# Optimization experiments

Hardware: AMD Instinct MI355X
Metric: run time of the kernel (lower is better)

Reference implementation:

```python
import jax, jax.numpy as jnp
import numpy as np

B, S, D = 2, 2048, 2048
H = 16
DH = D // H  # 128, head dim for q, also the single kv head dim
ROPE_BASE = 10000.0


def _rope_cos_sin(seq_len, dim, dtype):
    inv_freq = 1.0 / (ROPE_BASE ** (jnp.arange(0, dim, 2, dtype=jnp.float32) / dim))
    t = jnp.arange(seq_len, dtype=jnp.float32)
    freqs = jnp.outer(t, inv_freq)            # [S, dim/2]
    emb = jnp.concatenate([freqs, freqs], -1)  # [S, dim]
    return jnp.cos(emb).astype(dtype), jnp.sin(emb).astype(dtype)


def _rotate_half(x):
    x1, x2 = x[..., : x.shape[-1] // 2], x[..., x.shape[-1] // 2 :]
    return jnp.concatenate([-x2, x1], axis=-1)


def setup_inputs() -> dict:
    key = jax.random.key(0)
    ks = jax.random.split(key, 7)
    s = 0.02
    return {
        "x": jax.random.normal(ks[0], (B, S, D), jnp.float32),
        "q_weight": jax.random.normal(ks[1], (H * DH, D), jnp.float32) * s,
        "q_bias": jax.random.normal(ks[2], (H * DH,), jnp.float32) * s,
        "kv_weight": jax.random.normal(ks[3], (2 * DH, D), jnp.float32) * s,
        "kv_bias": jax.random.normal(ks[4], (2 * DH,), jnp.float32) * s,
        "o_weight": jax.random.normal(ks[5], (D, H * DH), jnp.float32) * s,
        "o_bias": jax.random.normal(ks[6], (D,), jnp.float32) * s,
    }


def reference(x, q_weight, q_bias, kv_weight, kv_bias, o_weight, o_bias):
    b, s, d = x.shape
    # fused-style MQA projections (torch F.linear: y = x @ W.T + b)
    q = x @ q_weight.T + q_bias                      # [B,S,H*DH]
    kv = x @ kv_weight.T + kv_bias                   # [B,S,2*DH]
    q = q.reshape(b, s, H, DH)
    k, v = kv[..., :DH], kv[..., DH:]                # [B,S,DH] single kv head

    # rotary embedding (GPT-NeoX / rotate_half style) on q and k
    cos, sin = _rope_cos_sin(s, DH, x.dtype)         # [S,DH]
    q = q * cos[None, :, None, :] + _rotate_half(q) * sin[None, :, None, :]
    k = k * cos[None, :, :] + _rotate_half(k) * sin[None, :, :]

    # causal MQA attention (flash_attn_varlen with full masks == dense causal)
    scale = 1.0 / jnp.sqrt(jnp.asarray(DH, x.dtype))
    scores = jnp.einsum("bqhd,bkd->bhqk", q, k) * scale   # [B,H,S,S]
    causal = jnp.tril(jnp.ones((s, s), bool))
    scores = jnp.where(causal[None, None], scores, jnp.asarray(-1e9, x.dtype))
    probs = jax.nn.softmax(scores, axis=-1)
    attn = jnp.einsum("bhqk,bkd->bqhd", probs, v)         # [B,S,H,DH]

    out = attn.reshape(b, s, H * DH) @ o_weight.T + o_bias
    return out
```

## Files before the change

kernel.cpp:

```cpp
#include <hip/hip_runtime.h>
#include <math.h>

constexpr int Bb  = 2;
constexpr int Ss  = 2048;
constexpr int Dd  = 2048;
constexpr int Hh  = 16;
constexpr int DHd = 128;
constexpr int BS  = Bb * Ss;
constexpr int NQKV = 2304;

typedef __bf16 bf16x8 __attribute__((ext_vector_type(8)));
typedef float  f32x4  __attribute__((ext_vector_type(4)));

static __device__ __forceinline__ unsigned short f2bf(float f) {
  union { float f; unsigned int u; } a; a.f = f;
  unsigned int u = a.u;
  unsigned int r = (u + 0x7fffu + ((u >> 16) & 1u)) >> 16;
  return (unsigned short)r;
}
static __device__ __forceinline__ float bf2f(unsigned short u) {
  union { unsigned int u; float f; } a; a.u = ((unsigned int)u) << 16;
  return a.f;
}
static __device__ __forceinline__ int cvtpk(float lo, float hi) {
  int r;
  asm("v_cvt_pk_bf16_f32 %0, %1, %2" : "=v"(r) : "v"(lo), "v"(hi));
  return r;
}
static __device__ __forceinline__ f32x4 mfma16(bf16x8 a, bf16x8 b, f32x4 c) {
  return __builtin_amdgcn_mfma_f32_16x16x32_bf16(a, b, c, 0, 0, 0);
}

__global__ __launch_bounds__(256) void cast_all(
    const float* __restrict__ qw, const float* __restrict__ kvw,
    const float* __restrict__ ow, const float* __restrict__ x,
    unsigned short* __restrict__ dst,
    float2* __restrict__ ctab)
{
  const int blk = blockIdx.x;
  if (blk >= 16896) {
    const int id = (blk - 16896) * 256 + threadIdx.x;
    const int s = id >> 6, i = id & 63;
    const float invf = exp2f(-(float)i * (13.287712379549449f / 64.0f));
    const float ang = (float)s * invf;
    ctab[id] = make_float2(cosf(ang), sinf(ang));
    return;
  }
  const int i = blk * 256 + threadIdx.x;
  const float* src; int off;
  if (i < 1048576)      { src = qw;  off = 0; }
  else if (i < 1179648) { src = kvw; off = 1048576; }
  else if (i < 2228224) { src = ow;  off = 1179648; }
  else                  { src = x;   off = 2228224; }
  const float4 v = ((const float4*)src)[i - off];
  ushort4 o;
  o.x = f2bf(v.x); o.y = f2bf(v.y); o.z = f2bf(v.z); o.w = f2bf(v.w);
  ((ushort4*)dst)[i] = o;
}

#define TM 128
#define TN 128
#define TK 32

#define GLOAD16(gp, lp)                                                        \
  __builtin_amdgcn_global_load_lds(                                            \
      (const __attribute__((address_space(1))) void*)(gp),                     \
      (__attribute__((address_space(3))) void*)(lp), 16, 0, 0)

template <bool BF16OUT>
__global__ __launch_bounds__(256) void gemm_bt_mfma(
    const unsigned short* __restrict__ A,
    const unsigned short* __restrict__ Bw,
    const float* __restrict__ bias1,
    const float* __restrict__ bias2,
    int nsplit,
    void* __restrict__ Cv,
    int M, int N, int K)
{
  __shared__ unsigned short As[TM * TK];
  __shared__ unsigned short Bs[TN * TK];

  const int tid  = threadIdx.x;
  const int w    = tid >> 6;
  const int lane = tid & 63;
  const int m0   = blockIdx.y * TM;
  const int n0   = blockIdx.x * TN;
  const int wm   = (w >> 1) * 64;
  const int wn   = (w & 1) * 64;

  f32x4 acc[4][4];
#pragma unroll
  for (int i = 0; i < 4; i++)
#pragma unroll
    for (int j = 0; j < 4; j++) acc[i][j] = (f32x4){0.f, 0.f, 0.f, 0.f};

  const int srow = lane >> 2;
  const int scol = (lane & 3) * 8;
  const unsigned short* aG0 = A  + (size_t)(m0 +      w * 16 + srow) * K + scol;
  const unsigned short* aG1 = A  + (size_t)(m0 + 64 + w * 16 + srow) * K + scol;
  const unsigned short* bG0 = Bw + (size_t)(n0 +      w * 16 + srow) * K + scol;
  const unsigned short* bG1 = Bw + (size_t)(n0 + 64 + w * 16 + srow) * K + scol;
  unsigned short* aL0 = &As[(     w * 16) * TK];
  unsigned short* aL1 = &As[(64 + w * 16) * TK];
  unsigned short* bL0 = &Bs[(     w * 16) * TK];
  unsigned short* bL1 = &Bs[(64 + w * 16) * TK];

  const int fr = lane & 15;
  const int fk = (lane >> 4) * 8;

  for (int k0 = 0; k0 < K; k0 += TK) {
    __syncthreads();
    GLOAD16(aG0 + k0, aL0);
    GLOAD16(aG1 + k0, aL1);
    GLOAD16(bG0 + k0, bL0);
    GLOAD16(bG1 + k0, bL1);
    __syncthreads();

    bf16x8 af[4], bfr[4];
#pragma unroll
    for (int i = 0; i < 4; i++)
      af[i] = *(const bf16x8*)&As[(wm + i * 16 + fr) * TK + fk];
#pragma unroll
    for (int j = 0; j < 4; j++)
      bfr[j] = *(const bf16x8*)&Bs[(wn + j * 16 + fr) * TK + fk];
#pragma unroll
    for (int i = 0; i < 4; i++)
#pragma unroll
      for (int j = 0; j < 4; j++)
        acc[i][j] = mfma16(af[i], bfr[j], acc[i][j]);
  }

  const int er = (lane >> 4) * 4;
  const int ec = lane & 15;
#pragma unroll
  for (int j = 0; j < 4; j++) {
    const int col = n0 + wn + j * 16 + ec;
    const float bv = (col < nsplit) ? bias1[col] : bias2[col - nsplit];
#pragma unroll
    for (int i = 0; i < 4; i++) {
      const int rbase = m0 + wm + i * 16 + er;
#pragma unroll
      for (int r = 0; r < 4; r++) {
        const float v = acc[i][j][r] + bv;
        if constexpr (BF16OUT)
          ((unsigned short*)Cv)[(size_t)(rbase + r) * N + col] = f2bf(v);
        else
          ((float*)Cv)[(size_t)(rbase + r) * N + col] = v;
      }
    }
  }
}

__global__ __launch_bounds__(256) void prep_kv(
    const unsigned short* __restrict__ QKV,
    const float2* __restrict__ ctab,
    unsigned short* __restrict__ Kb,
    unsigned short* __restrict__ Vt)
{
  __shared__ unsigned short Vtile[64 * 136];

  const int blk = blockIdx.x;
  const int b   = blk >> 5;
  const int s0  = (blk & 31) * 64;
  const int t   = threadIdx.x;

  {
    const int r = t >> 2, p = t & 3;
    const int row = blk * 64 + r;
    const int s = row & (Ss - 1);
    const unsigned short* src = QKV + (size_t)row * NQKV + 2048 + p * 16;
    const float2* ct = ctab + s * 64 + p * 16;
    union { uint4 v[2]; unsigned short a[16]; } lo, hi, ol, oh;
    lo.v[0] = *(const uint4*)src;        lo.v[1] = *(const uint4*)(src + 8);
    hi.v[0] = *(const uint4*)(src + 64); hi.v[1] = *(const uint4*)(src + 72);
#pragma unroll
    for (int e = 0; e < 16; e++) {
      const float2 cs = ct[e];
      const float l = bf2f(lo.a[e]), hh = bf2f(hi.a[e]);
      ol.a[e] = f2bf(l * cs.x - hh * cs.y);
      oh.a[e] = f2bf(hh * cs.x + l * cs.y);
    }
    unsigned short* dst = Kb + (size_t)row * 128 + p * 16;
    *(uint4*)dst        = ol.v[0]; *(uint4*)(dst + 8)  = ol.v[1];
    *(uint4*)(dst + 64) = oh.v[0]; *(uint4*)(dst + 72) = oh.v[1];
  }

#pragma unroll
  for (int c = 0; c < 4; c++) {
    const int id = c * 256 + t;
    const int vr = id >> 4, cc = id & 15;
    *(uint4*)&Vtile[vr * 136 + cc * 8] =
        *(const uint4*)(QKV + (size_t)(blk * 64 + vr) * NQKV + 2176 + cc * 8);
  }
  __syncthreads();

  {
    const int d = t >> 1, half = t & 1;
    union { uint4 v[4]; unsigned short a[32]; } val;
#pragma unroll
    for (int kk = 0; kk < 32; kk++)
      val.a[kk] = Vtile[(half * 32 + kk) * 136 + d];
    unsigned short* dst = Vt + ((size_t)(b * 128 + d)) * Ss + s0 + half * 32;
#pragma unroll
    for (int c = 0; c < 4; c++) *(uint4*)(dst + c * 8) = val.v[c];
  }
}

__global__ __launch_bounds__(256, 2) void flash_v11(
    const unsigned short* __restrict__ QKV,
    const unsigned short* __restrict__ Kb,
    const unsigned short* __restrict__ Vt,
    const float2* __restrict__ ctab,
    unsigned short* __restrict__ attn)
{
  __shared__ unsigned short Ks[4 * 128 * 32];
  __shared__ unsigned short Vs[4 * 128 * 32];

  const int g  = (int)blockIdx.x;
  const int lo = g & 255, hi = g >> 8;
  const int p  = hi ? (15 - (lo & 15)) : (lo & 15);
  const int hb = (lo >> 4) + 16 * hi;
  const int h  = hb & 15;
  const int b  = hb >> 4;

  const int qA0 = (31 - p) * 64;
  const int qB0 = p * 64;

  const int tid = threadIdx.x;
  const int w = tid >> 6, lane = tid & 63;
  const int lg = lane >> 4, lm = lane & 15;
  const int qrowA = qA0 + w * 16 + lm;
  const int qrowA_lo = qA0 + w * 16;
  const int qrowA_hi = qA0 + w * 16 + 15;
  const int qrowB = qB0 + w * 16 + lm;
  const int qrowB_lo = qB0 + w * 16;
  const int qrowB_hi = qB0 + w * 16 + 15;

  const int klg = lg ^ ((lm >> 1) & 3);

  const float sscale = 0.08838834764831845f * 1.4426950408889634f;

  bf16x8 qfA[4], qfB[4];
  {
    union U8 { bf16x8 v; unsigned short a[8]; };
#pragma unroll
    for (int tile = 0; tile < 2; tile++) {
      const int qrow = tile ? qrowB : qrowA;
      const unsigned short* qp =
          QKV + (size_t)(b * Ss + qrow) * NQKV + h * DHd + lg * 8;
      const float2* ct = ctab + qrow * 64 + lg * 8;
      U8 lo0, lo1, hi0, hi1, ol0, ol1, oh0, oh1;
      lo0.v = *(const bf16x8*)(qp);
      lo1.v = *(const bf16x8*)(qp + 32);
      hi0.v = *(const bf16x8*)(qp + 64);
      hi1.v = *(const bf16x8*)(qp + 96);
#pragma unroll
      for (int j = 0; j < 8; j++) {
        {
          const float2 cs = ct[j];
          const float l = bf2f(lo0.a[j]), hh = bf2f(hi0.a[j]);
          ol0.a[j] = f2bf((l * cs.x - hh * cs.y) * sscale);
          oh0.a[j] = f2bf((hh * cs.x + l * cs.y) * sscale);
        }
        {
          const float2 cs = ct[32 + j];
          const float l = bf2f(lo1.a[j]), hh = bf2f(hi1.a[j]);
          ol1.a[j] = f2bf((l * cs.x - hh * cs.y) * sscale);
          oh1.a[j] = f2bf((hh * cs.x + l * cs.y) * sscale);
        }
      }
      if (tile == 0) { qfA[0]=ol0.v; qfA[1]=ol1.v; qfA[2]=oh0.v; qfA[3]=oh1.v; }
      else           { qfB[0]=ol0.v; qfB[1]=ol1.v; qfB[2]=oh0.v; qfB[3]=oh1.v; }
    }
  }

  f32x4 otA[8], otB[8];
#pragma unroll
  for (int dt = 0; dt < 8; dt++) {
    otA[dt] = (f32x4){0.f, 0.f, 0.f, 0.f};
    otB[dt] = (f32x4){0.f, 0.f, 0.f, 0.f};
  }
  float lsumA = 0.f, lsumB = 0.f;

  const int sr  = lane >> 2;
  const int sc8 = ((lane & 3) ^ ((lane >> 3) & 3)) * 8;
  const unsigned short* kg =
      Kb + (size_t)b * Ss * 128 + (size_t)sr * 128 + w * 32 + sc8;
  const unsigned short* vg =
      Vt + (size_t)b * 128 * Ss + (size_t)(w * 32 + sr) * Ss + sc8;
  unsigned short* ksl = &Ks[w * 4096];

  const int addr0 = (2 * (lg & 1)) * 16 + lm;
  const int addr1 = addr0 + 16;
  const bool sel_hi = (lg & 2) != 0;

  auto half32 = [&](int keybase, int tA, const unsigned short* VsP,
                    const bf16x8 (&qf)[4], f32x4 (&ot)[8], float& lsum,
                    int qrow, bool needmask) {
    f32x4 s[2];
    s[0] = (f32x4){0.f, 0.f, 0.f, 0.f};
    s[1] = (f32x4){0.f, 0.f, 0.f, 0.f};
    __builtin_amdgcn_s_setprio(1);
#pragma unroll
    for (int kf = 0; kf < 4; kf++) {
      const bf16x8 k0 = *(const bf16x8*)&Ks[kf * 4096 + ((tA)     * 16 + lm) * 32 + klg * 8];
      const bf16x8 k1 = *(const bf16x8*)&Ks[kf * 4096 + ((tA + 1) * 16 + lm) * 32 + klg * 8];
      s[0] = mfma16(k0, qf[kf], s[0]);
      s[1] = mfma16(k1, qf[kf], s[1]);
    }
    __builtin_amdgcn_s_setprio(0);
    int pk[2][2];
#pragma unroll
    for (int t = 0; t < 2; t++) {
      float pv[4];
#pragma unroll
      for (int r = 0; r < 4; r++) pv[r] = exp2f(s[t][r]);
      if (needmask) {
        const int kb = keybase + t * 16 + 4 * lg;
#pragma unroll
        for (int r = 0; r < 4; r++)
          if (kb + r > qrow) pv[r] = 0.f;
      }
#pragma unroll
      for (int r = 0; r < 4; r++) lsum += pv[r];
      pk[t][0] = cvtpk(pv[0], pv[1]);
      pk[t][1] = cvtpk(pv[2], pv[3]);
    }
    union { int d[4]; bf16x8 v; } pb;
#pragma unroll
    for (int d = 0; d < 4; d++) {
      const int src = (d < 2) ? addr0 : addr1;
      const int v0 = __shfl(pk[0][d & 1], src);
      const int v1 = __shfl(pk[1][d & 1], src);
      pb.d[d] = sel_hi ? v1 : v0;
    }
    __builtin_amdgcn_s_setprio(1);
#pragma unroll
    for (int dt = 0; dt < 8; dt++) {
      const bf16x8 vfrag = *(const bf16x8*)&VsP[(dt * 16 + lm) * 32 + klg * 8];
      ot[dt] = mfma16(vfrag, pb.v, ot[dt]);
    }
    __builtin_amdgcn_s_setprio(0);
  };

  for (int j0 = 0; j0 <= qA0; j0 += 128) {
    __syncthreads();
#pragma unroll
    for (int i = 0; i < 8; i++)
      GLOAD16(kg + (size_t)(j0 + i * 16) * 128, ksl + i * 512);
#pragma unroll
    for (int ks2 = 0; ks2 < 4; ks2++) {
      unsigned short* vsl = &Vs[ks2 * 4096 + (w * 32) * 32];
      GLOAD16(vg + j0 + ks2 * 32,                  vsl);
      GLOAD16(vg + (size_t)16 * Ss + j0 + ks2 * 32, vsl + 512);
    }
    __syncthreads();

#pragma unroll
    for (int t32 = 0; t32 < 4; t32++) {
      const int kb = j0 + t32 * 32;
      if (kb <= qrowA_hi)
        half32(kb, t32 * 2, &Vs[t32 * 4096], qfA, otA, lsumA, qrowA,
               kb + 31 > qrowA_lo);
    }
#pragma unroll
    for (int t32 = 0; t32 < 4; t32++) {
      const int kb = j0 + t32 * 32;
      if (kb <= qrowB_hi)
        half32(kb, t32 * 2, &Vs[t32 * 4096], qfB, otB, lsumB, qrowB,
               kb + 31 > qrowB_lo);
    }
  }

#pragma unroll
  for (int tile = 0; tile < 2; tile++) {
    float lsum = tile ? lsumB : lsumA;
    const int qrow = tile ? qrowB : qrowA;
    lsum += __shfl_xor(lsum, 16);
    lsum += __shfl_xor(lsum, 32);
    const float inv = 1.0f / lsum;
    unsigned short* dst =
        attn + (size_t)(b * Ss + qrow) * Dd + h * DHd + lg * 4;
#pragma unroll
    for (int dt = 0; dt < 8; dt++) {
      const f32x4 o = tile ? otB[dt] : otA[dt];
      uint2 st;
      st.x = (unsigned int)cvtpk(o[0] * inv, o[1] * inv);
      st.y = (unsigned int)cvtpk(o[2] * inv, o[3] * inv);
      *(uint2*)(dst + dt * 16) = st;
    }
  }
}

extern "C" void kernel_launch(void* const* d_in, const int* in_sizes, int n_in,
                              void* d_out, int out_size, void* d_ws, size_t ws_size,
                              hipStream_t stream) {
  const float* x   = (const float*)d_in[0];
  const float* qw  = (const float*)d_in[1];
  const float* qb  = (const float*)d_in[2];
  const float* kvw = (const float*)d_in[3];
  const float* kvb = (const float*)d_in[4];
  const float* ow  = (const float*)d_in[5];
  const float* ob  = (const float*)d_in[6];
  float* out = (float*)d_out;

  unsigned short* wsb    = (unsigned short*)d_ws;
  unsigned short* wqkv   = wsb;
  unsigned short* owb    = wsb + 4718592;
  unsigned short* xb     = wsb + 8912896;
  unsigned short* attn_b = xb;
  unsigned short* QKV    = wsb + 17301504;
  unsigned short* Kb     = wsb + 26738688;
  unsigned short* Vt     = wsb + 27262976;
  float2*         ctab   = (float2*)(wsb + 27787264);

  cast_all<<<17408, 256, 0, stream>>>(qw, kvw, ow, x, wqkv, ctab);

  gemm_bt_mfma<true><<<dim3(NQKV / TN, BS / TM), 256, 0, stream>>>(
      xb, wqkv, qb, kvb, 2048, QKV, BS, NQKV, Dd);

  prep_kv<<<BS / 64, 256, 0, stream>>>(QKV, ctab, Kb, Vt);

  flash_v11<<<512, 256, 0, stream>>>(QKV, Kb, Vt, ctab, attn_b);

  gemm_bt_mfma<false><<<dim3(Dd / TN, BS / TM), 256, 0, stream>>>(
      attn_b, owb, ob, ob, Dd, out, BS, Dd, Dd);
}
```

Measured before the change: 304.3 us.

## Double-buffer K/V tiles in flash attention with 64-key prefetch pipeline

Splits the attention key loop into 64-key tiles held in two shared-memory buffers. The next tile's K and V global-to-LDS loads are issued right after the barrier, so they overlap with the MFMA work on the current tile, and each iteration needs one barrier instead of two. A new tile64_2 path handles both 32-key halves together, with four score MFMAs interleaved per k-fragment, and falls back to half32 on the diagonal edge. In exchange the loop runs twice as many iterations, shared-memory use and register pressure go up, and correctness depends on the barrier also waiting for the outstanding loads.

```diff
diff --git a/kernel.cpp b/kernel.cpp
--- a/kernel.cpp
+++ b/kernel.cpp
@@ -206,15 +206,15 @@
   }
 }
 
-__global__ __launch_bounds__(256, 2) void flash_v11(
+__global__ __launch_bounds__(256, 2) void flash_v12(
     const unsigned short* __restrict__ QKV,
     const unsigned short* __restrict__ Kb,
     const unsigned short* __restrict__ Vt,
     const float2* __restrict__ ctab,
     unsigned short* __restrict__ attn)
 {
-  __shared__ unsigned short Ks[4 * 128 * 32];
-  __shared__ unsigned short Vs[4 * 128 * 32];
+  __shared__ unsigned short Ks[2 * 8192];
+  __shared__ unsigned short Vs[2 * 8192];
 
   const int g  = (int)blockIdx.x;
   const int lo = g & 255, hi = g >> 8;
@@ -288,27 +288,41 @@
       Kb + (size_t)b * Ss * 128 + (size_t)sr * 128 + w * 32 + sc8;
   const unsigned short* vg =
       Vt + (size_t)b * 128 * Ss + (size_t)(w * 32 + sr) * Ss + sc8;
-  unsigned short* ksl = &Ks[w * 4096];
+
+  auto stage = [&](int bi, int jj) {
+    unsigned short* ksl  = &Ks[bi * 8192 + w * 2048];
+    unsigned short* vsl0 = &Vs[bi * 8192 + (w * 32) * 32];
+    unsigned short* vsl1 = &Vs[bi * 8192 + 4096 + (w * 32) * 32];
+#pragma unroll
+    for (int i = 0; i < 4; i++)
+      GLOAD16(kg + (size_t)(jj + i * 16) * 128, ksl + i * 512);
+#pragma unroll
+    for (int i = 0; i < 2; i++) {
+      GLOAD16(vg + (size_t)(i * 16) * Ss + jj,      vsl0 + i * 512);
+      GLOAD16(vg + (size_t)(i * 16) * Ss + jj + 32, vsl1 + i * 512);
+    }
+  };
 
   const int addr0 = (2 * (lg & 1)) * 16 + lm;
   const int addr1 = addr0 + 16;
   const bool sel_hi = (lg & 2) != 0;
 
-  auto half32 = [&](int keybase, int tA, const unsigned short* VsP,
-                    const bf16x8 (&qf)[4], f32x4 (&ot)[8], float& lsum,
-                    int qrow, bool needmask) {
+  auto half32 = [&](const unsigned short* KsB, const unsigned short* VsB,
+                    int keybase, const bf16x8 (&qf)[4], f32x4 (&ot)[8],
+                    float& lsum, int qrow, int qrow_lo) {
     f32x4 s[2];
     s[0] = (f32x4){0.f, 0.f, 0.f, 0.f};
     s[1] = (f32x4){0.f, 0.f, 0.f, 0.f};
     __builtin_amdgcn_s_setprio(1);
 #pragma unroll
     for (int kf = 0; kf < 4; kf++) {
-      const bf16x8 k0 = *(const bf16x8*)&Ks[kf * 4096 + ((tA)     * 16 + lm) * 32 + klg * 8];
-      const bf16x8 k1 = *(const bf16x8*)&Ks[kf * 4096 + ((tA + 1) * 16 + lm) * 32 + klg * 8];
+      const bf16x8 k0 = *(const bf16x8*)&KsB[kf * 2048 + (      lm) * 32 + klg * 8];
+      const bf16x8 k1 = *(const bf16x8*)&KsB[kf * 2048 + (16 + lm) * 32 + klg * 8];
       s[0] = mfma16(k0, qf[kf], s[0]);
       s[1] = mfma16(k1, qf[kf], s[1]);
     }
     __builtin_amdgcn_s_setprio(0);
+    const bool needmask = keybase + 31 > qrow_lo;
     int pk[2][2];
 #pragma unroll
     for (int t = 0; t < 2; t++) {
@@ -337,39 +351,98 @@
     __builtin_amdgcn_s_setprio(1);
 #pragma unroll
     for (int dt = 0; dt < 8; dt++) {
-      const bf16x8 vfrag = *(const bf16x8*)&VsP[(dt * 16 + lm) * 32 + klg * 8];
-      ot[dt] = mfma16(vfrag, pb.v, ot[dt]);
+      const bf16x8 vf = *(const bf16x8*)&VsB[(dt * 16 + lm) * 32 + klg * 8];
+      ot[dt] = mfma16(vf, pb.v, ot[dt]);
     }
     __builtin_amdgcn_s_setprio(0);
   };
 
-  for (int j0 = 0; j0 <= qA0; j0 += 128) {
+  auto tile64_2 = [&](const unsigned short* KsB, const unsigned short* VsB,
+                      int keybase, const bf16x8 (&qf)[4], f32x4 (&ot)[8],
+                      float& lsum, int qrow, int qrow_lo) {
+    f32x4 s[2][2];
+#pragma unroll
+    for (int hf = 0; hf < 2; hf++) {
+      s[hf][0] = (f32x4){0.f, 0.f, 0.f, 0.f};
+      s[hf][1] = (f32x4){0.f, 0.f, 0.f, 0.f};
+    }
+    __builtin_amdgcn_s_setprio(1);
+#pragma unroll
+    for (int kf = 0; kf < 4; kf++) {
+      const bf16x8 k00 = *(const bf16x8*)&KsB[kf * 2048 + (      lm) * 32 + klg * 8];
+      const bf16x8 k01 = *(const bf16x8*)&KsB[kf * 2048 + (16 + lm) * 32 + klg * 8];
+      const bf16x8 k10 = *(const bf16x8*)&KsB[kf * 2048 + (32 + lm) * 32 + klg * 8];
+      const bf16x8 k11 = *(const bf16x8*)&KsB[kf * 2048 + (48 + lm) * 32 + klg * 8];
+      s[0][0] = mfma16(k00, qf[kf], s[0][0]);
+      s[0][1] = mfma16(k01, qf[kf], s[0][1]);
+      s[1][0] = mfma16(k10, qf[kf], s[1][0]);
+      s[1][1] = mfma16(k11, qf[kf], s[1][1]);
+    }
+    __builtin_amdgcn_s_setprio(0);
+    int pk[2][2][2];
+#pragma unroll
+    for (int hf = 0; hf < 2; hf++) {
+      const bool needmask = keybase + hf * 32 + 31 > qrow_lo;
+#pragma unroll
+      for (int t = 0; t < 2; t++) {
+        float pv[4];
+#pragma unroll
+        for (int r = 0; r < 4; r++) pv[r] = exp2f(s[hf][t][r]);
+        if (needmask) {
+          const int kb = keybase + hf * 32 + t * 16 + 4 * lg;
+#pragma unroll
+          for (int r = 0; r < 4; r++)
+            if (kb + r > qrow) pv[r] = 0.f;
+        }
+#pragma unroll
+        for (int r = 0; r < 4; r++) lsum += pv[r];
+        pk[hf][t][0] = cvtpk(pv[0], pv[1]);
+        pk[hf][t][1] = cvtpk(pv[2], pv[3]);
+      }
+    }
+    union { int d[4]; bf16x8 v; } pb[2];
+#pragma unroll
+    for (int hf = 0; hf < 2; hf++) {
+#pragma unroll
+      for (int d = 0; d < 4; d++) {
+        const int src = (d < 2) ? addr0 : addr1;
+        const int v0 = __shfl(pk[hf][0][d & 1], src);
+        const int v1 = __shfl(pk[hf][1][d & 1], src);
+        pb[hf].d[d] = sel_hi ? v1 : v0;
+      }
+    }
+    __builtin_amdgcn_s_setprio(1);
+#pragma unroll
+    for (int dt = 0; dt < 8; dt++) {
+      const bf16x8 vf0 = *(const bf16x8*)&VsB[       (dt * 16 + lm) * 32 + klg * 8];
+      const bf16x8 vf1 = *(const bf16x8*)&VsB[4096 + (dt * 16 + lm) * 32 + klg * 8];
+      ot[dt] = mfma16(vf0, pb[0].v, ot[dt]);
+      ot[dt] = mfma16(vf1, pb[1].v, ot[dt]);
+    }
+    __builtin_amdgcn_s_setprio(0);
+  };
+
+  stage(0, 0);
+  int cur = 0;
+  for (int j0 = 0; j0 <= qA0; j0 += 64) {
     __syncthreads();
-#pragma unroll
-    for (int i = 0; i < 8; i++)
-      GLOAD16(kg + (size_t)(j0 + i * 16) * 128, ksl + i * 512);
-#pragma unroll
-    for (int ks2 = 0; ks2 < 4; ks2++) {
-      unsigned short* vsl = &Vs[ks2 * 4096 + (w * 32) * 32];
-      GLOAD16(vg + j0 + ks2 * 32,                  vsl);
-      GLOAD16(vg + (size_t)16 * Ss + j0 + ks2 * 32, vsl + 512);
-    }
-    __syncthreads();
-
-#pragma unroll
-    for (int t32 = 0; t32 < 4; t32++) {
-      const int kb = j0 + t32 * 32;
-      if (kb <= qrowA_hi)
-        half32(kb, t32 * 2, &Vs[t32 * 4096], qfA, otA, lsumA, qrowA,
-               kb + 31 > qrowA_lo);
-    }
-#pragma unroll
-    for (int t32 = 0; t32 < 4; t32++) {
-      const int kb = j0 + t32 * 32;
-      if (kb <= qrowB_hi)
-        half32(kb, t32 * 2, &Vs[t32 * 4096], qfB, otB, lsumB, qrowB,
-               kb + 31 > qrowB_lo);
-    }
+    if (j0 + 64 <= qA0) stage(cur ^ 1, j0 + 64);
+
+    const unsigned short* KsB = &Ks[cur * 8192];
+    const unsigned short* VsB = &Vs[cur * 8192];
+
+    if (j0 + 32 <= qrowA_hi)
+      tile64_2(KsB, VsB, j0, qfA, otA, lsumA, qrowA, qrowA_lo);
+    else
+      half32(KsB, VsB, j0, qfA, otA, lsumA, qrowA, qrowA_lo);
+
+    if (j0 <= qrowB_hi) {
+      if (j0 + 32 <= qrowB_hi)
+        tile64_2(KsB, VsB, j0, qfB, otB, lsumB, qrowB, qrowB_lo);
+      else
+        half32(KsB, VsB, j0, qfB, otB, lsumB, qrowB, qrowB_lo);
+    }
+    cur ^= 1;
   }
 
 #pragma unroll
@@ -421,7 +494,7 @@
 
   prep_kv<<<BS / 64, 256, 0, stream>>>(QKV, ctab, Kb, Vt);
 
-  flash_v11<<<512, 256, 0, stream>>>(QKV, Kb, Vt, ctab, attn_b);
+  flash_v12<<<512, 256, 0, stream>>>(QKV, Kb, Vt, ctab, attn_b);
 
   gemm_bt_mfma<false><<<dim3(Dd / TN, BS / TM), 256, 0, stream>>>(
       attn_b, owb, ob, ob, Dd, out, BS, Dd, Dd);
```

New measurement: 305.4 us. Within noise of the previous version (+0.4%).

## Split paired query tiles across separate waves in 512-thread flash blocks

Applied to the files above, without the earlier changes.

The flash attention kernel now launches 512 threads per block: waves 0-3 handle the high query tile A and waves 4-7 handle the low tile B, where before each wave processed both tiles serially. K tile loads are done by A-waves and V tile loads by B-waves, with the shared-memory layout unchanged. Each wave now holds one set of accumulators, which cuts register pressure and doubles resident waves for latency hiding. B-waves exit their work early on the causal mask but still wait at every block barrier, so they sit idle while A-waves keep computing.

```diff
diff --git a/kernel.cpp b/kernel.cpp
--- a/kernel.cpp
+++ b/kernel.cpp
@@ -206,7 +206,7 @@
   }
 }
 
-__global__ __launch_bounds__(256, 2) void flash_v11(
+__global__ __launch_bounds__(512, 4) void flash_v13(
     const unsigned short* __restrict__ QKV,
     const unsigned short* __restrict__ Kb,
     const unsigned short* __restrict__ Vt,
@@ -229,74 +229,68 @@
   const int tid = threadIdx.x;
   const int w = tid >> 6, lane = tid & 63;
   const int lg = lane >> 4, lm = lane & 15;
-  const int qrowA = qA0 + w * 16 + lm;
-  const int qrowA_lo = qA0 + w * 16;
-  const int qrowA_hi = qA0 + w * 16 + 15;
-  const int qrowB = qB0 + w * 16 + lm;
-  const int qrowB_lo = qB0 + w * 16;
-  const int qrowB_hi = qB0 + w * 16 + 15;
+
+  const bool isA = (w < 4);
+  const int sw = w & 3;
+  const int qt0 = isA ? qA0 : qB0;
+  const int qrow    = qt0 + sw * 16 + lm;
+  const int qrow_lo = qt0 + sw * 16;
+  const int qrow_hi = qt0 + sw * 16 + 15;
 
   const int klg = lg ^ ((lm >> 1) & 3);
 
   const float sscale = 0.08838834764831845f * 1.4426950408889634f;
 
-  bf16x8 qfA[4], qfB[4];
+  bf16x8 qf[4];
   {
     union U8 { bf16x8 v; unsigned short a[8]; };
-#pragma unroll
-    for (int tile = 0; tile < 2; tile++) {
-      const int qrow = tile ? qrowB : qrowA;
-      const unsigned short* qp =
-          QKV + (size_t)(b * Ss + qrow) * NQKV + h * DHd + lg * 8;
-      const float2* ct = ctab + qrow * 64 + lg * 8;
-      U8 lo0, lo1, hi0, hi1, ol0, ol1, oh0, oh1;
-      lo0.v = *(const bf16x8*)(qp);
-      lo1.v = *(const bf16x8*)(qp + 32);
-      hi0.v = *(const bf16x8*)(qp + 64);
-      hi1.v = *(const bf16x8*)(qp + 96);
-#pragma unroll
-      for (int j = 0; j < 8; j++) {
-        {
-          const float2 cs = ct[j];
-          const float l = bf2f(lo0.a[j]), hh = bf2f(hi0.a[j]);
-          ol0.a[j] = f2bf((l * cs.x - hh * cs.y) * sscale);
-          oh0.a[j] = f2bf((hh * cs.x + l * cs.y) * sscale);
-        }
-        {
-          const float2 cs = ct[32 + j];
-          const float l = bf2f(lo1.a[j]), hh = bf2f(hi1.a[j]);
-          ol1.a[j] = f2bf((l * cs.x - hh * cs.y) * sscale);
-          oh1.a[j] = f2bf((hh * cs.x + l * cs.y) * sscale);
-        }
+    const unsigned short* qp =
+        QKV + (size_t)(b * Ss + qrow) * NQKV + h * DHd + lg * 8;
+    const float2* ct = ctab + qrow * 64 + lg * 8;
+    U8 lo0, lo1, hi0, hi1, ol0, ol1, oh0, oh1;
+    lo0.v = *(const bf16x8*)(qp);
+    lo1.v = *(const bf16x8*)(qp + 32);
+    hi0.v = *(const bf16x8*)(qp + 64);
+    hi1.v = *(const bf16x8*)(qp + 96);
+#pragma unroll
+    for (int j = 0; j < 8; j++) {
+      {
+        const float2 cs = ct[j];
+        const float l = bf2f(lo0.a[j]), hh = bf2f(hi0.a[j]);
+        ol0.a[j] = f2bf((l * cs.x - hh * cs.y) * sscale);
+        oh0.a[j] = f2bf((hh * cs.x + l * cs.y) * sscale);
       }
-      if (tile == 0) { qfA[0]=ol0.v; qfA[1]=ol1.v; qfA[2]=oh0.v; qfA[3]=oh1.v; }
-      else           { qfB[0]=ol0.v; qfB[1]=ol1.v; qfB[2]=oh0.v; qfB[3]=oh1.v; }
-    }
-  }
-
-  f32x4 otA[8], otB[8];
-#pragma unroll
-  for (int dt = 0; dt < 8; dt++) {
-    otA[dt] = (f32x4){0.f, 0.f, 0.f, 0.f};
-    otB[dt] = (f32x4){0.f, 0.f, 0.f, 0.f};
-  }
-  float lsumA = 0.f, lsumB = 0.f;
+      {
+        const float2 cs = ct[32 + j];
+        const float l = bf2f(lo1.a[j]), hh = bf2f(hi1.a[j]);
+        ol1.a[j] = f2bf((l * cs.x - hh * cs.y) * sscale);
+        oh1.a[j] = f2bf((hh * cs.x + l * cs.y) * sscale);
+      }
+    }
+    qf[0] = ol0.v; qf[1] = ol1.v; qf[2] = oh0.v; qf[3] = oh1.v;
+  }
+
+  f32x4 ot[8];
+#pragma unroll
+  for (int dt = 0; dt < 8; dt++) ot[dt] = (f32x4){0.f, 0.f, 0.f, 0.f};
+  float lsum = 0.f;
 
   const int sr  = lane >> 2;
   const int sc8 = ((lane & 3) ^ ((lane >> 3) & 3)) * 8;
   const unsigned short* kg =
-      Kb + (size_t)b * Ss * 128 + (size_t)sr * 128 + w * 32 + sc8;
+      Kb + (size_t)b * Ss * 128 + (size_t)sr * 128 + (w & 3) * 32 + sc8;
+  unsigned short* ksl = &Ks[(w & 3) * 4096];
+  const int vks = w & 3;
   const unsigned short* vg =
-      Vt + (size_t)b * 128 * Ss + (size_t)(w * 32 + sr) * Ss + sc8;
-  unsigned short* ksl = &Ks[w * 4096];
+      Vt + (size_t)b * 128 * Ss + (size_t)sr * Ss + sc8;
+  unsigned short* vsl = &Vs[vks * 4096];
 
   const int addr0 = (2 * (lg & 1)) * 16 + lm;
   const int addr1 = addr0 + 16;
   const bool sel_hi = (lg & 2) != 0;
 
   auto half32 = [&](int keybase, int tA, const unsigned short* VsP,
-                    const bf16x8 (&qf)[4], f32x4 (&ot)[8], float& lsum,
-                    int qrow, bool needmask) {
+                    bool needmask) {
     f32x4 s[2];
     s[0] = (f32x4){0.f, 0.f, 0.f, 0.f};
     s[1] = (f32x4){0.f, 0.f, 0.f, 0.f};
@@ -345,50 +339,36 @@
 
   for (int j0 = 0; j0 <= qA0; j0 += 128) {
     __syncthreads();
-#pragma unroll
-    for (int i = 0; i < 8; i++)
-      GLOAD16(kg + (size_t)(j0 + i * 16) * 128, ksl + i * 512);
-#pragma unroll
-    for (int ks2 = 0; ks2 < 4; ks2++) {
-      unsigned short* vsl = &Vs[ks2 * 4096 + (w * 32) * 32];
-      GLOAD16(vg + j0 + ks2 * 32,                  vsl);
-      GLOAD16(vg + (size_t)16 * Ss + j0 + ks2 * 32, vsl + 512);
+    if (isA) {
+#pragma unroll
+      for (int i = 0; i < 8; i++)
+        GLOAD16(kg + (size_t)(j0 + i * 16) * 128, ksl + i * 512);
+    } else {
+#pragma unroll
+      for (int i = 0; i < 8; i++)
+        GLOAD16(vg + (size_t)(i * 16) * Ss + j0 + vks * 32, vsl + i * 512);
     }
     __syncthreads();
 
 #pragma unroll
     for (int t32 = 0; t32 < 4; t32++) {
       const int kb = j0 + t32 * 32;
-      if (kb <= qrowA_hi)
-        half32(kb, t32 * 2, &Vs[t32 * 4096], qfA, otA, lsumA, qrowA,
-               kb + 31 > qrowA_lo);
-    }
-#pragma unroll
-    for (int t32 = 0; t32 < 4; t32++) {
-      const int kb = j0 + t32 * 32;
-      if (kb <= qrowB_hi)
-        half32(kb, t32 * 2, &Vs[t32 * 4096], qfB, otB, lsumB, qrowB,
-               kb + 31 > qrowB_lo);
-    }
-  }
-
-#pragma unroll
-  for (int tile = 0; tile < 2; tile++) {
-    float lsum = tile ? lsumB : lsumA;
-    const int qrow = tile ? qrowB : qrowA;
-    lsum += __shfl_xor(lsum, 16);
-    lsum += __shfl_xor(lsum, 32);
-    const float inv = 1.0f / lsum;
-    unsigned short* dst =
-        attn + (size_t)(b * Ss + qrow) * Dd + h * DHd + lg * 4;
-#pragma unroll
-    for (int dt = 0; dt < 8; dt++) {
-      const f32x4 o = tile ? otB[dt] : otA[dt];
-      uint2 st;
-      st.x = (unsigned int)cvtpk(o[0] * inv, o[1] * inv);
-      st.y = (unsigned int)cvtpk(o[2] * inv, o[3] * inv);
-      *(uint2*)(dst + dt * 16) = st;
-    }
+      if (kb <= qrow_hi)
+        half32(kb, t32 * 2, &Vs[t32 * 4096], kb + 31 > qrow_lo);
+    }
+  }
+
+  lsum += __shfl_xor(lsum, 16);
+  lsum += __shfl_xor(lsum, 32);
+  const float inv = 1.0f / lsum;
+  unsigned short* dst =
+      attn + (size_t)(b * Ss + qrow) * Dd + h * DHd + lg * 4;
+#pragma unroll
+  for (int dt = 0; dt < 8; dt++) {
+    uint2 st;
+    st.x = (unsigned int)cvtpk(ot[dt][0] * inv, ot[dt][1] * inv);
+    st.y = (unsigned int)cvtpk(ot[dt][2] * inv, ot[dt][3] * inv);
+    *(uint2*)(dst + dt * 16) = st;
   }
 }
 
@@ -421,7 +401,7 @@
 
   prep_kv<<<BS / 64, 256, 0, stream>>>(QKV, ctab, Kb, Vt);
 
-  flash_v11<<<512, 256, 0, stream>>>(QKV, Kb, Vt, ctab, attn_b);
+  flash_v13<<<512, 512, 0, stream>>>(QKV, Kb, Vt, ctab, attn_b);
 
   gemm_bt_mfma<false><<<dim3(Dd / TN, BS / TM), 256, 0, stream>>>(
       attn_b, owb, ob, ob, Dd, out, BS, Dd, Dd);
```

New measurement: 304.7 us. Within noise of the previous version (+0.1%).
